# Performance work log

Measured on AMD Instinct MI355X. Metric: run time of the kernel, lower is better.

The kernel has to match this reference:

```python
import jax, jax.numpy as jnp
import numpy as np

N_SPOT, N_CITY, N_WORD = 20000, 2000, 20000
E_HAS, E_IN, E_DESC, E_RDESC = 100000, 100000, 400000, 400000
HID = 256


def setup_inputs() -> dict:
    key = jax.random.key(0)
    ks = jax.random.split(key, 48)

    def g(i, shape, s):
        return jax.random.normal(ks[i], shape, dtype=jnp.float32) * s

    inp = {}
    inp['x_spot'] = g(0, (N_SPOT, 2560), 0.5)
    inp['x_city'] = g(1, (N_CITY, 128), 0.5)
    inp['x_word'] = g(2, (N_WORD, 300), 0.5)
    inp['W_att'] = g(3, (4, 512, 128), 0.05)  # 4 heads, per_dim=128
    inp['q_att'] = g(4, (4, 128), 0.1)
    i = 5
    for n, d in [('w1_has_s', 128), ('w1_has_t', 512), ('w1_in_s', 512), ('w1_in_t', 128),
                 ('w1_desc_s', 300), ('w1_desc_t', 512), ('w1_rdesc_s', 512), ('w1_rdesc_t', 300)]:
        inp[n] = g(i, (d, HID), 0.05); i += 1
    for n in ['w2_has_s', 'w2_has_t', 'w2_in_s', 'w2_in_t', 'w2_desc_s', 'w2_desc_t', 'w2_rdesc_s', 'w2_rdesc_t']:
        inp[n] = g(i, (HID, HID), 0.05); i += 1
    for n in ['wl_spot', 'wl_city', 'wl_word']:
        inp[n] = g(i, (HID, 1), 0.05); i += 1
    for n in ['bl_spot', 'bl_city', 'bl_word']:
        inp[n] = jnp.zeros((1,), jnp.float32)
    for n, e, hi in [('e_has_src', E_HAS, N_CITY), ('e_has_tgt', E_HAS, N_SPOT),
                     ('e_in_src', E_IN, N_SPOT), ('e_in_tgt', E_IN, N_CITY),
                     ('e_desc_src', E_DESC, N_WORD), ('e_desc_tgt', E_DESC, N_SPOT),
                     ('e_rdesc_src', E_RDESC, N_SPOT), ('e_rdesc_tgt', E_RDESC, N_WORD)]:
        inp[n] = jax.random.randint(ks[i], (e,), 0, hi, dtype=jnp.int32); i += 1
    return inp


def _attention(x, W_att, q_att):
    # AttentionModule(input_dim=512, num_heads=4, split=5): (N, 2560) -> (N, 512)
    x = x.reshape(-1, 5, 512)
    xw = jnp.einsum('nsi,hio->hnso', x, W_att)                      # (4,N,5,128)
    a = jax.nn.leaky_relu(jnp.einsum('hnso,ho->hns', xw, q_att), 0.2)
    a = jax.nn.softmax(a, axis=2)                                   # softmax over split dim
    out = jnp.einsum('hnso,hns->hno', xw, a)                        # (4,N,128)
    return jnp.transpose(out, (1, 0, 2)).reshape(x.shape[0], 4 * 128)


def _scatter_mean(src, idx, n):
    s = jax.ops.segment_sum(src, idx, num_segments=n)
    c = jax.ops.segment_sum(jnp.ones((src.shape[0], 1), src.dtype), idx, num_segments=n)
    return s / jnp.maximum(c, 1.0)


def _edge(x_s, x_t, w_s, w_t, src, tgt):
    # per-edge-type linear, gather on source index, scatter-mean into targets
    msg = (x_s @ w_s)[src]
    return x_t @ w_t + _scatter_mean(msg, tgt, x_t.shape[0])


def _conv(xs, xc, xw, w, e):
    spot = _edge(xc, xs, w['has_s'], w['has_t'], e['has_src'], e['has_tgt']) \
         + _edge(xw, xs, w['desc_s'], w['desc_t'], e['desc_src'], e['desc_tgt'])
    city = _edge(xs, xc, w['in_s'], w['in_t'], e['in_src'], e['in_tgt'])
    word = _edge(xs, xw, w['rdesc_s'], w['rdesc_t'], e['rdesc_src'], e['rdesc_tgt'])
    # div[spot]=2, div[city]=div[word]=1; ReLU flag applies a second (idempotent) relu
    return jax.nn.relu(spot * 0.5), jax.nn.relu(city), jax.nn.relu(word)


def reference(x_spot, x_city, x_word, W_att, q_att,
              w1_has_s, w1_has_t, w1_in_s, w1_in_t, w1_desc_s, w1_desc_t, w1_rdesc_s, w1_rdesc_t,
              w2_has_s, w2_has_t, w2_in_s, w2_in_t, w2_desc_s, w2_desc_t, w2_rdesc_s, w2_rdesc_t,
              wl_spot, bl_spot, wl_city, bl_city, wl_word, bl_word,
              e_has_src, e_has_tgt, e_in_src, e_in_tgt, e_desc_src, e_desc_tgt, e_rdesc_src, e_rdesc_tgt):
    e = dict(has_src=e_has_src, has_tgt=e_has_tgt, in_src=e_in_src, in_tgt=e_in_tgt,
             desc_src=e_desc_src, desc_tgt=e_desc_tgt, rdesc_src=e_rdesc_src, rdesc_tgt=e_rdesc_tgt)
    w1 = dict(has_s=w1_has_s, has_t=w1_has_t, in_s=w1_in_s, in_t=w1_in_t,
              desc_s=w1_desc_s, desc_t=w1_desc_t, rdesc_s=w1_rdesc_s, rdesc_t=w1_rdesc_t)
    w2 = dict(has_s=w2_has_s, has_t=w2_has_t, in_s=w2_in_s, in_t=w2_in_t,
              desc_s=w2_desc_s, desc_t=w2_desc_t, rdesc_s=w2_rdesc_s, rdesc_t=w2_rdesc_t)
    xs = _attention(x_spot, W_att, q_att)  # multi=True path
    s1, c1, wd1 = _conv(xs, x_city, x_word, w1, e)
    s2, c2, wd2 = _conv(s1, c1, wd1, w2, e)
    out_spot = s2 @ wl_spot + bl_spot
    out_city = c2 @ wl_city + bl_city
    out_word = wd2 @ wl_word + bl_word
    # concat=True: mean over the two layer outputs per node type
    return ((s1 + s2) * 0.5, (c1 + c2) * 0.5, (wd1 + wd2) * 0.5, out_spot, out_city, out_word)
```

## Files before the change

kernel.cpp:

```cpp
#include <hip/hip_runtime.h>
#include <hip/hip_bf16.h>

#define HID 256
#define NSPOT 20000
#define NCITY 2000
#define NWORD 20000

typedef __attribute__((ext_vector_type(8))) short bhalf8;
typedef __attribute__((ext_vector_type(4))) float floatx4;
typedef __attribute__((ext_vector_type(8))) unsigned short ushortx8;

__device__ inline float bf2f(unsigned short u) {
    union { unsigned int i; float f; } v; v.i = (unsigned int)u << 16; return v.f;
}
__device__ inline unsigned short f2bf(float f) {
    __hip_bfloat16 b = __float2bfloat16(f);
    return *reinterpret_cast<unsigned short*>(&b);
}
__device__ inline float4 ld4(const float* p, size_t off) {
    return *reinterpret_cast<const float4*>(p + off);
}

__global__ void wq_kernel(const float* __restrict__ W, const float* __restrict__ q,
                          float* __restrict__ wq) {
    int idx = blockIdx.x * 256 + threadIdx.x;
    if (idx >= 2048) return;
    int h = idx >> 9, i = idx & 511;
    const float* Wr = W + ((size_t)h * 512 + i) * 128;
    const float* qr = q + h * 128;
    float s = 0.f;
    #pragma unroll 4
    for (int o = 0; o < 128; o++) s += Wr[o] * qr[o];
    wq[idx] = s;
}

__global__ __launch_bounds__(256) void attn_kernel(const float* __restrict__ x,
                                                   const float* __restrict__ wq,
                                                   __hip_bfloat16* __restrict__ xbar) {
    __shared__ float xl[2560];
    __shared__ float al[4][8];
    int n = blockIdx.x;
    int tid = threadIdx.x;
    int wave = tid >> 6, lane = tid & 63;
    const float4* xr4 = (const float4*)(x + (size_t)n * 2560);
    for (int i = tid; i < 640; i += 256) ((float4*)xl)[i] = xr4[i];
    __syncthreads();
    const float* wqh = wq + wave * 512;
    for (int s = 0; s < 5; s++) {
        float a = 0.f;
        #pragma unroll
        for (int j = 0; j < 8; j++)
            a += xl[s * 512 + lane + j * 64] * wqh[lane + j * 64];
        #pragma unroll
        for (int off = 32; off > 0; off >>= 1) a += __shfl_down(a, off, 64);
        if (lane == 0) al[wave][s] = a;
    }
    __syncthreads();
    if (tid < 4) {
        float z[5]; float m = -1e30f;
        #pragma unroll
        for (int s = 0; s < 5; s++) {
            float v = al[tid][s];
            v = (v >= 0.f) ? v : 0.2f * v;
            z[s] = v; m = fmaxf(m, v);
        }
        float e[5]; float sum = 0.f;
        #pragma unroll
        for (int s = 0; s < 5; s++) { e[s] = __expf(z[s] - m); sum += e[s]; }
        float r = 1.f / sum;
        #pragma unroll
        for (int s = 0; s < 5; s++) al[tid][s] = e[s] * r;
    }
    __syncthreads();
    float a0 = al[wave][0], a1 = al[wave][1], a2 = al[wave][2], a3 = al[wave][3], a4 = al[wave][4];
    __hip_bfloat16* xo = xbar + ((size_t)wave * NSPOT + n) * 512;
    #pragma unroll
    for (int j = 0; j < 8; j++) {
        int i = lane + j * 64;
        float v = a0 * xl[i] + a1 * xl[512 + i] + a2 * xl[1024 + i] + a3 * xl[1536 + i] + a4 * xl[2048 + i];
        xo[i] = __float2bfloat16(v);
    }
}

#define KP 40
struct GemmDesc {
    const __hip_bfloat16* A;
    const __hip_bfloat16* Bt;
    float* C;
    __hip_bfloat16* Cb;
    int lda, ldb, ldc, ldcb, M, K, N;
};
struct GemmDesc8 { GemmDesc d[8]; };

__global__ __launch_bounds__(256) void gemm_grouped(GemmDesc8 descs) {
    GemmDesc g = descs.d[blockIdx.z];
    int rowbase = blockIdx.x * 128;
    int colbase = blockIdx.y * 128;
    if (rowbase >= g.M || colbase >= g.N) return;
    __shared__ short As[128 * KP];
    __shared__ short Bs[128 * KP];
    int tid = threadIdx.x;
    int wave = tid >> 6, lane = tid & 63;
    int wr = wave & 1, wc = wave >> 1;
    int quad = lane >> 4, l16 = lane & 15;
    int srow = tid >> 2;
    int skoff = (tid & 3) * 8;
    const __hip_bfloat16* A = g.A;
    const __hip_bfloat16* Bt = g.Bt;
    int lda = g.lda, ldb = g.ldb, M = g.M, K = g.K;
    floatx4 acc[4][4];
    #pragma unroll
    for (int i = 0; i < 4; i++)
        #pragma unroll
        for (int j = 0; j < 4; j++)
            acc[i][j] = (floatx4){0.f, 0.f, 0.f, 0.f};

    for (int k0 = 0; k0 < K; k0 += 32) {
        #pragma unroll
        for (int i = 0; i < 2; i++) {
            int r = srow + i * 64;
            int gr = rowbase + r;
            int4 va = make_int4(0, 0, 0, 0);
            if (gr < M) va = *(const int4*)(A + (size_t)gr * lda + k0 + skoff);
            *(int4*)(As + r * KP + skoff) = va;
            int4 vb = *(const int4*)(Bt + (size_t)(colbase + r) * ldb + k0 + skoff);
            *(int4*)(Bs + r * KP + skoff) = vb;
        }
        __syncthreads();
        bhalf8 af[4], bfr[4];
        #pragma unroll
        for (int rt = 0; rt < 4; rt++)
            af[rt] = *(const bhalf8*)(As + (wr * 64 + rt * 16 + l16) * KP + quad * 8);
        #pragma unroll
        for (int ct = 0; ct < 4; ct++)
            bfr[ct] = *(const bhalf8*)(Bs + (wc * 64 + ct * 16 + l16) * KP + quad * 8);
        #pragma unroll
        for (int rt = 0; rt < 4; rt++)
            #pragma unroll
            for (int ct = 0; ct < 4; ct++)
                acc[rt][ct] = __builtin_amdgcn_mfma_f32_16x16x32_bf16(af[rt], bfr[ct], acc[rt][ct], 0, 0, 0);
        __syncthreads();
    }
    #pragma unroll
    for (int rt = 0; rt < 4; rt++) {
        #pragma unroll
        for (int r = 0; r < 4; r++) {
            int grow = rowbase + wr * 64 + rt * 16 + quad * 4 + r;
            if (grow < M) {
                #pragma unroll
                for (int ct = 0; ct < 4; ct++) {
                    int gcol = colbase + wc * 64 + ct * 16 + l16;
                    float v = acc[rt][ct][r];
                    if (g.C)  g.C[(size_t)grow * g.ldc + gcol] = v;
                    if (g.Cb) g.Cb[(size_t)grow * g.ldcb + gcol] = __float2bfloat16(v);
                }
            }
        }
    }
}

struct TDesc { const float* in; const float* in2; __hip_bfloat16* out; int K; int N; int Kp; };
struct TDesc8 { TDesc d[8]; };
__global__ void transpose_cast_kernel(TDesc8 descs) {
    TDesc dsc = descs.d[blockIdx.z];
    __shared__ float tile[32][33];
    int k0 = blockIdx.x * 32, n0 = blockIdx.y * 32;
    if (k0 >= dsc.Kp || n0 >= dsc.N) return;
    int tn = threadIdx.x & 31, t8 = threadIdx.x >> 5;
    #pragma unroll
    for (int i = 0; i < 4; i++) {
        int k = k0 + t8 * 4 + i;
        float v = 0.f;
        if (k < dsc.K && n0 + tn < dsc.N) {
            v = dsc.in[(size_t)k * dsc.N + n0 + tn];
            if (dsc.in2) v += dsc.in2[(size_t)k * dsc.N + n0 + tn];
        }
        tile[t8 * 4 + i][tn] = v;
    }
    __syncthreads();
    int kk = threadIdx.x & 31, n8 = threadIdx.x >> 5;
    #pragma unroll
    for (int i = 0; i < 4; i++) {
        int n = n0 + n8 * 4 + i;
        int k = k0 + kk;
        if (n < dsc.N && k < dsc.Kp)
            dsc.out[(size_t)n * dsc.Kp + k] = __float2bfloat16(tile[kk][n8 * 4 + i]);
    }
}

__global__ void cast_kernel(const float* __restrict__ in, __hip_bfloat16* __restrict__ out, int n) {
    int i = blockIdx.x * 256 + threadIdx.x;
    if (i < n) out[i] = __float2bfloat16(in[i]);
}

__global__ void cast_pad_kernel(const float* __restrict__ in, __hip_bfloat16* __restrict__ out,
                                int rows, int K, int Kp) {
    int idx = blockIdx.x * 256 + threadIdx.x;
    if (idx >= rows * Kp) return;
    int r = idx / Kp, k = idx - r * Kp;
    out[idx] = (k < K) ? __float2bfloat16(in[(size_t)r * K + k]) : __float2bfloat16(0.f);
}

struct EdgeDesc { const int* src; const int* tgt; int E; int n;
                  int* deg; int* rp; int* cur; int* cs; };
struct EdgeDesc4 { EdgeDesc d[4]; };

__global__ void hist4_kernel(EdgeDesc4 ds) {
    EdgeDesc d = ds.d[blockIdx.y];
    int e = blockIdx.x * 256 + threadIdx.x;
    if (e < d.E) atomicAdd(&d.deg[d.tgt[e]], 1);
}

__global__ void scan4_kernel(EdgeDesc4 ds) {
    EdgeDesc dd = ds.d[blockIdx.x];
    __shared__ int partx[257];
    __shared__ int part[256];
    int tid = threadIdx.x;
    int n = dd.n;
    int chunk = (n + 255) / 256;
    int lo = tid * chunk;
    int hi = lo + chunk; if (hi > n) hi = n;
    int s = 0;
    for (int i = lo; i < hi; i++) s += dd.deg[i];
    part[tid] = s;
    __syncthreads();
    if (tid == 0) {
        int acc = 0;
        for (int i = 0; i < 256; i++) { partx[i] = acc; acc += part[i]; }
        partx[256] = acc;
    }
    __syncthreads();
    int acc = partx[tid];
    for (int i = lo; i < hi; i++) { dd.rp[i] = acc; dd.cur[i] = acc; acc += dd.deg[i]; }
    if (tid == 0) dd.rp[n] = partx[256];
}

__global__ void fill4_kernel(EdgeDesc4 ds) {
    EdgeDesc d = ds.d[blockIdx.y];
    int e = blockIdx.x * 256 + threadIdx.x;
    if (e >= d.E) return;
    int t = d.tgt[e];
    int pos = atomicAdd(&d.cur[t], 1);
    d.cs[pos] = d.src[e];
}

__device__ inline void seg_mean8(const __hip_bfloat16* __restrict__ msg,
                                 const int* __restrict__ rp, const int* __restrict__ cs,
                                 int t, int half, int li, float a[8]) {
    int lo = rp[t], hi = rp[t + 1];
    #pragma unroll
    for (int j = 0; j < 8; j++) a[j] = 0.f;
    int col = li * 8;
    int i = lo + half;
    for (; i + 6 < hi; i += 8) {
        int s0 = cs[i], s1 = cs[i + 2], s2 = cs[i + 4], s3 = cs[i + 6];
        ushortx8 u0 = *(const ushortx8*)(msg + (size_t)s0 * HID + col);
        ushortx8 u1 = *(const ushortx8*)(msg + (size_t)s1 * HID + col);
        ushortx8 u2 = *(const ushortx8*)(msg + (size_t)s2 * HID + col);
        ushortx8 u3 = *(const ushortx8*)(msg + (size_t)s3 * HID + col);
        #pragma unroll
        for (int k = 0; k < 8; k++)
            a[k] += (bf2f(u0[k]) + bf2f(u1[k])) + (bf2f(u2[k]) + bf2f(u3[k]));
    }
    for (; i < hi; i += 2) {
        int s0 = cs[i];
        ushortx8 u = *(const ushortx8*)(msg + (size_t)s0 * HID + col);
        #pragma unroll
        for (int k = 0; k < 8; k++) a[k] += bf2f(u[k]);
    }
    #pragma unroll
    for (int j = 0; j < 8; j++) a[j] += __shfl_down(a[j], 32, 64);
    float inv = 1.f / fmaxf((float)(hi - lo), 1.f);
    #pragma unroll
    for (int j = 0; j < 8; j++) a[j] *= inv;
}

__global__ __launch_bounds__(256) void fused_ac1_kernel(
    const __hip_bfloat16* __restrict__ Phas,   const int* __restrict__ rp_has,   const int* __restrict__ cs_has,
    const __hip_bfloat16* __restrict__ Pdesc,  const int* __restrict__ rp_desc,  const int* __restrict__ cs_desc,
    const __hip_bfloat16* __restrict__ Pin,    const int* __restrict__ rp_in,    const int* __restrict__ cs_in,
    const __hip_bfloat16* __restrict__ Prdesc, const int* __restrict__ rp_rdesc, const int* __restrict__ cs_rdesc,
    const float* __restrict__ Ss, const float* __restrict__ Sc, const float* __restrict__ Sw,
    __hip_bfloat16* __restrict__ s1b, __hip_bfloat16* __restrict__ c1b,
    __hip_bfloat16* __restrict__ wd1b) {
    int row = blockIdx.x * 4 + (threadIdx.x >> 6);
    if (row >= NSPOT + NCITY + NWORD) return;
    int lane = threadIdx.x & 63;
    int half = lane >> 5, li = lane & 31;
    float v[8]; __hip_bfloat16* ob; size_t off;
    if (row < NSPOT) {
        float mh[8], md[8];
        seg_mean8(Phas, rp_has, cs_has, row, half, li, mh);
        seg_mean8(Pdesc, rp_desc, cs_desc, row, half, li, md);
        off = (size_t)row * HID + li * 8;
        float4 sa = ld4(Ss, off), sb = ld4(Ss, off + 4);
        v[0] = fmaxf((sa.x + mh[0] + md[0]) * 0.5f, 0.f);
        v[1] = fmaxf((sa.y + mh[1] + md[1]) * 0.5f, 0.f);
        v[2] = fmaxf((sa.z + mh[2] + md[2]) * 0.5f, 0.f);
        v[3] = fmaxf((sa.w + mh[3] + md[3]) * 0.5f, 0.f);
        v[4] = fmaxf((sb.x + mh[4] + md[4]) * 0.5f, 0.f);
        v[5] = fmaxf((sb.y + mh[5] + md[5]) * 0.5f, 0.f);
        v[6] = fmaxf((sb.z + mh[6] + md[6]) * 0.5f, 0.f);
        v[7] = fmaxf((sb.w + mh[7] + md[7]) * 0.5f, 0.f);
        ob = s1b;
    } else if (row < NSPOT + NCITY) {
        int r = row - NSPOT;
        float mi[8];
        seg_mean8(Pin, rp_in, cs_in, r, half, li, mi);
        off = (size_t)r * HID + li * 8;
        float4 sa = ld4(Sc, off), sb = ld4(Sc, off + 4);
        v[0] = fmaxf(sa.x + mi[0], 0.f); v[1] = fmaxf(sa.y + mi[1], 0.f);
        v[2] = fmaxf(sa.z + mi[2], 0.f); v[3] = fmaxf(sa.w + mi[3], 0.f);
        v[4] = fmaxf(sb.x + mi[4], 0.f); v[5] = fmaxf(sb.y + mi[5], 0.f);
        v[6] = fmaxf(sb.z + mi[6], 0.f); v[7] = fmaxf(sb.w + mi[7], 0.f);
        ob = c1b;
    } else {
        int r = row - NSPOT - NCITY;
        float mr[8];
        seg_mean8(Prdesc, rp_rdesc, cs_rdesc, r, half, li, mr);
        off = (size_t)r * HID + li * 8;
        float4 sa = ld4(Sw, off), sb = ld4(Sw, off + 4);
        v[0] = fmaxf(sa.x + mr[0], 0.f); v[1] = fmaxf(sa.y + mr[1], 0.f);
        v[2] = fmaxf(sa.z + mr[2], 0.f); v[3] = fmaxf(sa.w + mr[3], 0.f);
        v[4] = fmaxf(sb.x + mr[4], 0.f); v[5] = fmaxf(sb.y + mr[5], 0.f);
        v[6] = fmaxf(sb.z + mr[6], 0.f); v[7] = fmaxf(sb.w + mr[7], 0.f);
        ob = wd1b;
    }
    if (half == 0) {
        ushortx8 ub;
        #pragma unroll
        for (int j = 0; j < 8; j++) ub[j] = f2bf(v[j]);
        *reinterpret_cast<ushortx8*>((unsigned short*)ob + off) = ub;
    }
}

__global__ __launch_bounds__(256) void fused_finale_kernel(
    const __hip_bfloat16* __restrict__ Phas,   const int* __restrict__ rp_has,   const int* __restrict__ cs_has,
    const __hip_bfloat16* __restrict__ Pdesc,  const int* __restrict__ rp_desc,  const int* __restrict__ cs_desc,
    const __hip_bfloat16* __restrict__ Pin,    const int* __restrict__ rp_in,    const int* __restrict__ cs_in,
    const __hip_bfloat16* __restrict__ Prdesc, const int* __restrict__ rp_rdesc, const int* __restrict__ cs_rdesc,
    const float* __restrict__ Ss, const float* __restrict__ Sc, const float* __restrict__ Sw,
    const __hip_bfloat16* __restrict__ s1b, const __hip_bfloat16* __restrict__ c1b,
    const __hip_bfloat16* __restrict__ wd1b,
    float* __restrict__ out0, const float* __restrict__ wls, const float* __restrict__ bls, float* __restrict__ out3,
    float* __restrict__ out1, const float* __restrict__ wlc, const float* __restrict__ blc, float* __restrict__ out4,
    float* __restrict__ out2, const float* __restrict__ wlw, const float* __restrict__ blw, float* __restrict__ out5) {
    int row = blockIdx.x * 4 + (threadIdx.x >> 6);
    if (row >= NSPOT + NCITY + NWORD) return;
    int lane = threadIdx.x & 63;
    int half = lane >> 5, li = lane & 31;
    float v[8]; const __hip_bfloat16* pl; const float* wl; const float* bl;
    float* om; float* od;
    int r; size_t off;
    if (row < NSPOT) {
        r = row;
        float mh[8], md[8];
        seg_mean8(Phas, rp_has, cs_has, r, half, li, mh);
        seg_mean8(Pdesc, rp_desc, cs_desc, r, half, li, md);
        off = (size_t)r * HID + li * 8;
        float4 sa = ld4(Ss, off), sb = ld4(Ss, off + 4);
        v[0] = fmaxf((sa.x + mh[0] + md[0]) * 0.5f, 0.f);
        v[1] = fmaxf((sa.y + mh[1] + md[1]) * 0.5f, 0.f);
        v[2] = fmaxf((sa.z + mh[2] + md[2]) * 0.5f, 0.f);
        v[3] = fmaxf((sa.w + mh[3] + md[3]) * 0.5f, 0.f);
        v[4] = fmaxf((sb.x + mh[4] + md[4]) * 0.5f, 0.f);
        v[5] = fmaxf((sb.y + mh[5] + md[5]) * 0.5f, 0.f);
        v[6] = fmaxf((sb.z + mh[6] + md[6]) * 0.5f, 0.f);
        v[7] = fmaxf((sb.w + mh[7] + md[7]) * 0.5f, 0.f);
        pl = s1b; wl = wls; bl = bls; om = out0; od = out3;
    } else if (row < NSPOT + NCITY) {
        r = row - NSPOT;
        float mi[8];
        seg_mean8(Pin, rp_in, cs_in, r, half, li, mi);
        off = (size_t)r * HID + li * 8;
        float4 sa = ld4(Sc, off), sb = ld4(Sc, off + 4);
        v[0] = fmaxf(sa.x + mi[0], 0.f); v[1] = fmaxf(sa.y + mi[1], 0.f);
        v[2] = fmaxf(sa.z + mi[2], 0.f); v[3] = fmaxf(sa.w + mi[3], 0.f);
        v[4] = fmaxf(sb.x + mi[4], 0.f); v[5] = fmaxf(sb.y + mi[5], 0.f);
        v[6] = fmaxf(sb.z + mi[6], 0.f); v[7] = fmaxf(sb.w + mi[7], 0.f);
        pl = c1b; wl = wlc; bl = blc; om = out1; od = out4;
    } else {
        r = row - NSPOT - NCITY;
        float mr[8];
        seg_mean8(Prdesc, rp_rdesc, cs_rdesc, r, half, li, mr);
        off = (size_t)r * HID + li * 8;
        float4 sa = ld4(Sw, off), sb = ld4(Sw, off + 4);
        v[0] = fmaxf(sa.x + mr[0], 0.f); v[1] = fmaxf(sa.y + mr[1], 0.f);
        v[2] = fmaxf(sa.z + mr[2], 0.f); v[3] = fmaxf(sa.w + mr[3], 0.f);
        v[4] = fmaxf(sb.x + mr[4], 0.f); v[5] = fmaxf(sb.y + mr[5], 0.f);
        v[6] = fmaxf(sb.z + mr[6], 0.f); v[7] = fmaxf(sb.w + mr[7], 0.f);
        pl = wd1b; wl = wlw; bl = blw; om = out2; od = out5;
    }
    ushortx8 up = *(const ushortx8*)((const unsigned short*)pl + off);
    if (half == 0) {
        *reinterpret_cast<float4*>(om + off) =
            make_float4((bf2f(up[0]) + v[0]) * 0.5f, (bf2f(up[1]) + v[1]) * 0.5f,
                        (bf2f(up[2]) + v[2]) * 0.5f, (bf2f(up[3]) + v[3]) * 0.5f);
        *reinterpret_cast<float4*>(om + off + 4) =
            make_float4((bf2f(up[4]) + v[4]) * 0.5f, (bf2f(up[5]) + v[5]) * 0.5f,
                        (bf2f(up[6]) + v[6]) * 0.5f, (bf2f(up[7]) + v[7]) * 0.5f);
    }
    float4 wa = *reinterpret_cast<const float4*>(wl + li * 8);
    float4 wb = *reinterpret_cast<const float4*>(wl + li * 8 + 4);
    float s = v[0] * wa.x + v[1] * wa.y + v[2] * wa.z + v[3] * wa.w
            + v[4] * wb.x + v[5] * wb.y + v[6] * wb.z + v[7] * wb.w;
    s += __shfl_down(s, 16, 64);
    s += __shfl_down(s, 8, 64);
    s += __shfl_down(s, 4, 64);
    s += __shfl_down(s, 2, 64);
    s += __shfl_down(s, 1, 64);
    if (lane == 0) od[r] = s + bl[0];
}

extern "C" void kernel_launch(void* const* d_in, const int* in_sizes, int n_in,
                              void* d_out, int out_size, void* d_ws, size_t ws_size,
                              hipStream_t stream) {
    const float* x_spot   = (const float*)d_in[0];
    const float* x_city   = (const float*)d_in[1];
    const float* x_word   = (const float*)d_in[2];
    const float* W_att    = (const float*)d_in[3];
    const float* q_att    = (const float*)d_in[4];
    const float* w1[8] = { (const float*)d_in[5], (const float*)d_in[6], (const float*)d_in[7],
                           (const float*)d_in[8], (const float*)d_in[9], (const float*)d_in[10],
                           (const float*)d_in[11], (const float*)d_in[12] };
    const float* w2[8] = { (const float*)d_in[13], (const float*)d_in[14], (const float*)d_in[15],
                           (const float*)d_in[16], (const float*)d_in[17], (const float*)d_in[18],
                           (const float*)d_in[19], (const float*)d_in[20] };
    const float* wl_spot = (const float*)d_in[21];
    const float* wl_city = (const float*)d_in[22];
    const float* wl_word = (const float*)d_in[23];
    const float* bl_spot = (const float*)d_in[24];
    const float* bl_city = (const float*)d_in[25];
    const float* bl_word = (const float*)d_in[26];
    const int* e_has_src   = (const int*)d_in[27];
    const int* e_has_tgt   = (const int*)d_in[28];
    const int* e_in_src    = (const int*)d_in[29];
    const int* e_in_tgt    = (const int*)d_in[30];
    const int* e_desc_src  = (const int*)d_in[31];
    const int* e_desc_tgt  = (const int*)d_in[32];
    const int* e_rdesc_src = (const int*)d_in[33];
    const int* e_rdesc_tgt = (const int*)d_in[34];
    const int E_has   = in_sizes[27];
    const int E_in    = in_sizes[29];
    const int E_desc  = in_sizes[31];
    const int E_rdesc = in_sizes[33];

    float* out = (float*)d_out;
    float* wsf = (float*)d_ws;
    typedef __hip_bfloat16 bf;

    size_t o = 0;
    auto alloc = [&](size_t nfloats) { float* p = wsf + o; o += (nfloats + 15) & ~(size_t)15; return p; };
    float* wqb       = alloc(2048);
    bf* xs_bf        = (bf*)alloc((size_t)NSPOT * 512 / 2);
    bf* x_city_bf    = (bf*)alloc((size_t)NCITY * 128 / 2);
    bf* x_word_bf    = (bf*)alloc((size_t)NWORD * 320 / 2);
    bf* Wt_att       = (bf*)alloc((size_t)4 * 128 * 512 / 2);
    int Kp1[7] = {128, 512, 512, 128, 320, 512, 320};
    bf* Wt1[7];
    for (int i = 0; i < 7; i++) Wt1[i] = (bf*)alloc((size_t)256 * Kp1[i] / 2);
    bf* Wt2[7];
    for (int i = 0; i < 7; i++) Wt2[i] = (bf*)alloc((size_t)256 * 256 / 2);
    float* Ss = alloc((size_t)NSPOT * HID);
    float* Sc = alloc((size_t)NCITY * HID);
    float* Sw = alloc((size_t)NWORD * HID);
    size_t regX = o;
    bf* xbar_bf = (bf*)(wsf + regX);
    size_t ox = regX;
    auto allocX = [&](size_t nfloats) { float* p = wsf + ox; ox += (nfloats + 15) & ~(size_t)15; return p; };
    bf* P_has_bf   = (bf*)allocX((size_t)NCITY * HID / 2);
    bf* P_in_bf    = (bf*)allocX((size_t)NSPOT * HID / 2);
    bf* P_desc_bf  = (bf*)allocX((size_t)NWORD * HID / 2);
    bf* P_rdesc_bf = (bf*)allocX((size_t)NSPOT * HID / 2);
    bf* s1b = (bf*)allocX((size_t)NSPOT * HID / 2);
    bf* c1b = (bf*)allocX((size_t)NCITY * HID / 2);
    bf* wd1b = (bf*)allocX((size_t)NWORD * HID / 2);
    o = regX + (size_t)4 * NSPOT * 512 / 2;
    int* wsi = (int*)(wsf + o);
    size_t io = 0;
    int* deg_has    = wsi + io; io += NSPOT;
    int* deg_desc   = wsi + io; io += NSPOT;
    int* deg_in     = wsi + io; io += NCITY;
    int* deg_rdesc  = wsi + io; io += NWORD;
    size_t deg_bytes = io * sizeof(int);
    int* rp_has     = wsi + io; io += NSPOT + 1;
    int* rp_desc    = wsi + io; io += NSPOT + 1;
    int* rp_in      = wsi + io; io += NCITY + 1;
    int* rp_rdesc   = wsi + io; io += NWORD + 1;
    int* cur_has    = wsi + io; io += NSPOT + 1;
    int* cur_desc   = wsi + io; io += NSPOT + 1;
    int* cur_in     = wsi + io; io += NCITY + 1;
    int* cur_rdesc  = wsi + io; io += NWORD + 1;
    int* cs_has     = wsi + io; io += E_has;
    int* cs_desc    = wsi + io; io += E_desc;
    int* cs_in      = wsi + io; io += E_in;
    int* cs_rdesc   = wsi + io; io += E_rdesc;
    (void)ws_size; (void)n_in; (void)out_size;

    {
        TDesc8 t{};
        for (int i = 0; i < 4; i++)
            t.d[i] = TDesc{ W_att + (size_t)i * 512 * 128, nullptr,
                            Wt_att + (size_t)i * 128 * 512, 512, 128, 512 };
        hipLaunchKernelGGL(transpose_cast_kernel, dim3(16, 4, 4), dim3(256), 0, stream, t);
    }
    {
        TDesc8 t{};
        t.d[0] = TDesc{ w1[0], nullptr, Wt1[0], 128, 256, 128 };
        t.d[1] = TDesc{ w1[1], w1[5],   Wt1[1], 512, 256, 512 };
        t.d[2] = TDesc{ w1[2], nullptr, Wt1[2], 512, 256, 512 };
        t.d[3] = TDesc{ w1[3], nullptr, Wt1[3], 128, 256, 128 };
        t.d[4] = TDesc{ w1[4], nullptr, Wt1[4], 300, 256, 320 };
        t.d[5] = TDesc{ w1[6], nullptr, Wt1[5], 512, 256, 512 };
        t.d[6] = TDesc{ w1[7], nullptr, Wt1[6], 300, 256, 320 };
        hipLaunchKernelGGL(transpose_cast_kernel, dim3(16, 8, 8), dim3(256), 0, stream, t);
    }
    {
        TDesc8 t{};
        t.d[0] = TDesc{ w2[0], nullptr, Wt2[0], 256, 256, 256 };
        t.d[1] = TDesc{ w2[1], w2[5],   Wt2[1], 256, 256, 256 };
        t.d[2] = TDesc{ w2[2], nullptr, Wt2[2], 256, 256, 256 };
        t.d[3] = TDesc{ w2[3], nullptr, Wt2[3], 256, 256, 256 };
        t.d[4] = TDesc{ w2[4], nullptr, Wt2[4], 256, 256, 256 };
        t.d[5] = TDesc{ w2[6], nullptr, Wt2[5], 256, 256, 256 };
        t.d[6] = TDesc{ w2[7], nullptr, Wt2[6], 256, 256, 256 };
        hipLaunchKernelGGL(transpose_cast_kernel, dim3(8, 8, 8), dim3(256), 0, stream, t);
    }
    hipLaunchKernelGGL(cast_kernel, dim3((NCITY * 128 + 255) / 256), dim3(256), 0, stream,
                       x_city, x_city_bf, NCITY * 128);
    hipLaunchKernelGGL(cast_pad_kernel, dim3((NWORD * 320 + 255) / 256), dim3(256), 0, stream,
                       x_word, x_word_bf, NWORD, 300, 320);

    EdgeDesc4 ed;
    ed.d[0] = EdgeDesc{ e_has_src,   e_has_tgt,   E_has,   NSPOT, deg_has,   rp_has,   cur_has,   cs_has };
    ed.d[1] = EdgeDesc{ e_desc_src,  e_desc_tgt,  E_desc,  NSPOT, deg_desc,  rp_desc,  cur_desc,  cs_desc };
    ed.d[2] = EdgeDesc{ e_in_src,    e_in_tgt,    E_in,    NCITY, deg_in,    rp_in,    cur_in,    cs_in };
    ed.d[3] = EdgeDesc{ e_rdesc_src, e_rdesc_tgt, E_rdesc, NWORD, deg_rdesc, rp_rdesc, cur_rdesc, cs_rdesc };
    int Emax = E_has;
    if (E_desc > Emax) Emax = E_desc;
    if (E_in > Emax) Emax = E_in;
    if (E_rdesc > Emax) Emax = E_rdesc;
    hipMemsetAsync((void*)deg_has, 0, deg_bytes, stream);
    hipLaunchKernelGGL(hist4_kernel, dim3((Emax + 255) / 256, 4), dim3(256), 0, stream, ed);
    hipLaunchKernelGGL(scan4_kernel, dim3(4), dim3(256), 0, stream, ed);
    hipLaunchKernelGGL(fill4_kernel, dim3((Emax + 255) / 256, 4), dim3(256), 0, stream, ed);

    hipLaunchKernelGGL(wq_kernel, dim3(8), dim3(256), 0, stream, W_att, q_att, wqb);
    hipLaunchKernelGGL(attn_kernel, dim3(NSPOT), dim3(256), 0, stream, x_spot, wqb, xbar_bf);

    int gx = (NSPOT + 127) / 128;

    {
        GemmDesc8 gd{};
        for (int h = 0; h < 4; h++)
            gd.d[h] = GemmDesc{ xbar_bf + (size_t)h * NSPOT * 512, Wt_att + (size_t)h * 128 * 512,
                                nullptr, xs_bf + h * 128, 512, 512, 0, 512, NSPOT, 512, 128 };
        hipLaunchKernelGGL(gemm_grouped, dim3(gx, 1, 4), dim3(256), 0, stream, gd);
    }

    {
        GemmDesc8 gd{};
        gd.d[0] = GemmDesc{ x_city_bf, Wt1[0], nullptr, P_has_bf,   128, 128, 0, HID, NCITY, 128, HID };
        gd.d[1] = GemmDesc{ xs_bf,     Wt1[1], Ss,      nullptr,    512, 512, HID, 0, NSPOT, 512, HID };
        gd.d[2] = GemmDesc{ xs_bf,     Wt1[2], nullptr, P_in_bf,    512, 512, 0, HID, NSPOT, 512, HID };
        gd.d[3] = GemmDesc{ x_city_bf, Wt1[3], Sc,      nullptr,    128, 128, HID, 0, NCITY, 128, HID };
        gd.d[4] = GemmDesc{ x_word_bf, Wt1[4], nullptr, P_desc_bf,  320, 320, 0, HID, NWORD, 320, HID };
        gd.d[5] = GemmDesc{ xs_bf,     Wt1[5], nullptr, P_rdesc_bf, 512, 512, 0, HID, NSPOT, 512, HID };
        gd.d[6] = GemmDesc{ x_word_bf, Wt1[6], Sw,      nullptr,    320, 320, HID, 0, NWORD, 320, HID };
        gd.d[7].M = 0; gd.d[7].N = 0;
        hipLaunchKernelGGL(gemm_grouped, dim3(gx, 2, 8), dim3(256), 0, stream, gd);
    }

    int rows3 = NSPOT + NCITY + NWORD;
    hipLaunchKernelGGL(fused_ac1_kernel, dim3((rows3 + 3) / 4), dim3(256), 0, stream,
                       P_has_bf, rp_has, cs_has, P_desc_bf, rp_desc, cs_desc,
                       P_in_bf, rp_in, cs_in, P_rdesc_bf, rp_rdesc, cs_rdesc,
                       Ss, Sc, Sw, s1b, c1b, wd1b);

    {
        GemmDesc8 gd{};
        gd.d[0] = GemmDesc{ c1b,  Wt2[0], nullptr, P_has_bf,   HID, HID, 0, HID, NCITY, HID, HID };
        gd.d[1] = GemmDesc{ s1b,  Wt2[1], Ss,      nullptr,    HID, HID, HID, 0, NSPOT, HID, HID };
        gd.d[2] = GemmDesc{ s1b,  Wt2[2], nullptr, P_in_bf,    HID, HID, 0, HID, NSPOT, HID, HID };
        gd.d[3] = GemmDesc{ c1b,  Wt2[3], Sc,      nullptr,    HID, HID, HID, 0, NCITY, HID, HID };
        gd.d[4] = GemmDesc{ wd1b, Wt2[4], nullptr, P_desc_bf,  HID, HID, 0, HID, NWORD, HID, HID };
        gd.d[5] = GemmDesc{ s1b,  Wt2[5], nullptr, P_rdesc_bf, HID, HID, 0, HID, NSPOT, HID, HID };
        gd.d[6] = GemmDesc{ wd1b, Wt2[6], Sw,      nullptr,    HID, HID, HID, 0, NWORD, HID, HID };
        gd.d[7].M = 0; gd.d[7].N = 0;
        hipLaunchKernelGGL(gemm_grouped, dim3(gx, 2, 8), dim3(256), 0, stream, gd);
    }

    float* out0 = out;
    float* out1 = out + (size_t)NSPOT * HID;
    float* out2 = out1 + (size_t)NCITY * HID;
    float* out3 = out2 + (size_t)NWORD * HID;
    float* out4 = out3 + NSPOT;
    float* out5 = out4 + NCITY;
    hipLaunchKernelGGL(fused_finale_kernel, dim3((rows3 + 3) / 4), dim3(256), 0, stream,
                       P_has_bf, rp_has, cs_has, P_desc_bf, rp_desc, cs_desc,
                       P_in_bf, rp_in, cs_in, P_rdesc_bf, rp_rdesc, cs_rdesc,
                       Ss, Sc, Sw, s1b, c1b, wd1b,
                       out0, wl_spot, bl_spot, out3,
                       out1, wl_city, bl_city, out4,
                       out2, wl_word, bl_word, out5);
}
```

Baseline: 835.1 us.

## Merge weight transposes into one launch and rebalance grouped GEMM launches

The three weight transpose-cast launches are merged into a single launch with 18 descriptors. The city and word layer-1 GEMMs move into the attention-projection grouped GEMM, which does not depend on xs, so that launch is better filled and the following launch holds only the three spot GEMMs. P_has and P_desc move out of the aliased xbar region so they are not overwritten while xbar is still live. The GEMM tile loader now precomputes row pointers and clamps out-of-range A rows to M-1 instead of zero-filling them, which removes per-iteration branches and index math; the extra rows are never stored.

```diff
diff --git a/kernel.cpp b/kernel.cpp
--- a/kernel.cpp
+++ b/kernel.cpp
@@ -108,6 +108,19 @@
     const __hip_bfloat16* A = g.A;
     const __hip_bfloat16* Bt = g.Bt;
     int lda = g.lda, ldb = g.ldb, M = g.M, K = g.K;
+
+    int r0 = srow, r1 = srow + 64;
+    int gra0 = rowbase + r0; gra0 = gra0 < M ? gra0 : M - 1;
+    int gra1 = rowbase + r1; gra1 = gra1 < M ? gra1 : M - 1;
+    const __hip_bfloat16* Arow0 = A + (size_t)gra0 * lda + skoff;
+    const __hip_bfloat16* Arow1 = A + (size_t)gra1 * lda + skoff;
+    const __hip_bfloat16* Brow0 = Bt + (size_t)(colbase + r0) * ldb + skoff;
+    const __hip_bfloat16* Brow1 = Bt + (size_t)(colbase + r1) * ldb + skoff;
+    short* sA0 = As + r0 * KP + skoff;
+    short* sA1 = As + r1 * KP + skoff;
+    short* sB0 = Bs + r0 * KP + skoff;
+    short* sB1 = Bs + r1 * KP + skoff;
+
     floatx4 acc[4][4];
     #pragma unroll
     for (int i = 0; i < 4; i++)
@@ -116,16 +129,10 @@
             acc[i][j] = (floatx4){0.f, 0.f, 0.f, 0.f};
 
     for (int k0 = 0; k0 < K; k0 += 32) {
-        #pragma unroll
-        for (int i = 0; i < 2; i++) {
-            int r = srow + i * 64;
-            int gr = rowbase + r;
-            int4 va = make_int4(0, 0, 0, 0);
-            if (gr < M) va = *(const int4*)(A + (size_t)gr * lda + k0 + skoff);
-            *(int4*)(As + r * KP + skoff) = va;
-            int4 vb = *(const int4*)(Bt + (size_t)(colbase + r) * ldb + k0 + skoff);
-            *(int4*)(Bs + r * KP + skoff) = vb;
-        }
+        *(int4*)sA0 = *(const int4*)(Arow0 + k0);
+        *(int4*)sA1 = *(const int4*)(Arow1 + k0);
+        *(int4*)sB0 = *(const int4*)(Brow0 + k0);
+        *(int4*)sB1 = *(const int4*)(Brow1 + k0);
         __syncthreads();
         bhalf8 af[4], bfr[4];
         #pragma unroll
@@ -160,8 +167,8 @@
 }
 
 struct TDesc { const float* in; const float* in2; __hip_bfloat16* out; int K; int N; int Kp; };
-struct TDesc8 { TDesc d[8]; };
-__global__ void transpose_cast_kernel(TDesc8 descs) {
+struct TDesc18 { TDesc d[18]; };
+__global__ void transpose_cast_kernel(TDesc18 descs) {
     TDesc dsc = descs.d[blockIdx.z];
     __shared__ float tile[32][33];
     int k0 = blockIdx.x * 32, n0 = blockIdx.y * 32;
@@ -464,13 +471,13 @@
     float* Ss = alloc((size_t)NSPOT * HID);
     float* Sc = alloc((size_t)NCITY * HID);
     float* Sw = alloc((size_t)NWORD * HID);
+    bf* P_has_bf  = (bf*)alloc((size_t)NCITY * HID / 2);
+    bf* P_desc_bf = (bf*)alloc((size_t)NWORD * HID / 2);
     size_t regX = o;
     bf* xbar_bf = (bf*)(wsf + regX);
     size_t ox = regX;
     auto allocX = [&](size_t nfloats) { float* p = wsf + ox; ox += (nfloats + 15) & ~(size_t)15; return p; };
-    bf* P_has_bf   = (bf*)allocX((size_t)NCITY * HID / 2);
     bf* P_in_bf    = (bf*)allocX((size_t)NSPOT * HID / 2);
-    bf* P_desc_bf  = (bf*)allocX((size_t)NWORD * HID / 2);
     bf* P_rdesc_bf = (bf*)allocX((size_t)NSPOT * HID / 2);
     bf* s1b = (bf*)allocX((size_t)NSPOT * HID / 2);
     bf* c1b = (bf*)allocX((size_t)NCITY * HID / 2);
@@ -498,33 +505,25 @@
     (void)ws_size; (void)n_in; (void)out_size;
 
     {
-        TDesc8 t{};
+        TDesc18 t{};
         for (int i = 0; i < 4; i++)
             t.d[i] = TDesc{ W_att + (size_t)i * 512 * 128, nullptr,
                             Wt_att + (size_t)i * 128 * 512, 512, 128, 512 };
-        hipLaunchKernelGGL(transpose_cast_kernel, dim3(16, 4, 4), dim3(256), 0, stream, t);
-    }
-    {
-        TDesc8 t{};
-        t.d[0] = TDesc{ w1[0], nullptr, Wt1[0], 128, 256, 128 };
-        t.d[1] = TDesc{ w1[1], w1[5],   Wt1[1], 512, 256, 512 };
-        t.d[2] = TDesc{ w1[2], nullptr, Wt1[2], 512, 256, 512 };
-        t.d[3] = TDesc{ w1[3], nullptr, Wt1[3], 128, 256, 128 };
-        t.d[4] = TDesc{ w1[4], nullptr, Wt1[4], 300, 256, 320 };
-        t.d[5] = TDesc{ w1[6], nullptr, Wt1[5], 512, 256, 512 };
-        t.d[6] = TDesc{ w1[7], nullptr, Wt1[6], 300, 256, 320 };
-        hipLaunchKernelGGL(transpose_cast_kernel, dim3(16, 8, 8), dim3(256), 0, stream, t);
-    }
-    {
-        TDesc8 t{};
-        t.d[0] = TDesc{ w2[0], nullptr, Wt2[0], 256, 256, 256 };
-        t.d[1] = TDesc{ w2[1], w2[5],   Wt2[1], 256, 256, 256 };
-        t.d[2] = TDesc{ w2[2], nullptr, Wt2[2], 256, 256, 256 };
-        t.d[3] = TDesc{ w2[3], nullptr, Wt2[3], 256, 256, 256 };
-        t.d[4] = TDesc{ w2[4], nullptr, Wt2[4], 256, 256, 256 };
-        t.d[5] = TDesc{ w2[6], nullptr, Wt2[5], 256, 256, 256 };
-        t.d[6] = TDesc{ w2[7], nullptr, Wt2[6], 256, 256, 256 };
-        hipLaunchKernelGGL(transpose_cast_kernel, dim3(8, 8, 8), dim3(256), 0, stream, t);
+        t.d[4]  = TDesc{ w1[0], nullptr, Wt1[0], 128, 256, 128 };
+        t.d[5]  = TDesc{ w1[1], w1[5],   Wt1[1], 512, 256, 512 };
+        t.d[6]  = TDesc{ w1[2], nullptr, Wt1[2], 512, 256, 512 };
+        t.d[7]  = TDesc{ w1[3], nullptr, Wt1[3], 128, 256, 128 };
+        t.d[8]  = TDesc{ w1[4], nullptr, Wt1[4], 300, 256, 320 };
+        t.d[9]  = TDesc{ w1[6], nullptr, Wt1[5], 512, 256, 512 };
+        t.d[10] = TDesc{ w1[7], nullptr, Wt1[6], 300, 256, 320 };
+        t.d[11] = TDesc{ w2[0], nullptr, Wt2[0], 256, 256, 256 };
+        t.d[12] = TDesc{ w2[1], w2[5],   Wt2[1], 256, 256, 256 };
+        t.d[13] = TDesc{ w2[2], nullptr, Wt2[2], 256, 256, 256 };
+        t.d[14] = TDesc{ w2[3], nullptr, Wt2[3], 256, 256, 256 };
+        t.d[15] = TDesc{ w2[4], nullptr, Wt2[4], 256, 256, 256 };
+        t.d[16] = TDesc{ w2[6], nullptr, Wt2[5], 256, 256, 256 };
+        t.d[17] = TDesc{ w2[7], nullptr, Wt2[6], 256, 256, 256 };
+        hipLaunchKernelGGL(transpose_cast_kernel, dim3(16, 8, 18), dim3(256), 0, stream, t);
     }
     hipLaunchKernelGGL(cast_kernel, dim3((NCITY * 128 + 255) / 256), dim3(256), 0, stream,
                        x_city, x_city_bf, NCITY * 128);
@@ -555,20 +554,20 @@
         for (int h = 0; h < 4; h++)
             gd.d[h] = GemmDesc{ xbar_bf + (size_t)h * NSPOT * 512, Wt_att + (size_t)h * 128 * 512,
                                 nullptr, xs_bf + h * 128, 512, 512, 0, 512, NSPOT, 512, 128 };
-        hipLaunchKernelGGL(gemm_grouped, dim3(gx, 1, 4), dim3(256), 0, stream, gd);
+        gd.d[4] = GemmDesc{ x_city_bf, Wt1[0], nullptr, P_has_bf,  128, 128, 0, HID, NCITY, 128, HID };
+        gd.d[5] = GemmDesc{ x_city_bf, Wt1[3], Sc,      nullptr,   128, 128, HID, 0, NCITY, 128, HID };
+        gd.d[6] = GemmDesc{ x_word_bf, Wt1[4], nullptr, P_desc_bf, 320, 320, 0, HID, NWORD, 320, HID };
+        gd.d[7] = GemmDesc{ x_word_bf, Wt1[6], Sw,      nullptr,   320, 320, HID, 0, NWORD, 320, HID };
+        hipLaunchKernelGGL(gemm_grouped, dim3(gx, 2, 8), dim3(256), 0, stream, gd);
     }
 
     {
         GemmDesc8 gd{};
-        gd.d[0] = GemmDesc{ x_city_bf, Wt1[0], nullptr, P_has_bf,   128, 128, 0, HID, NCITY, 128, HID };
-        gd.d[1] = GemmDesc{ xs_bf,     Wt1[1], Ss,      nullptr,    512, 512, HID, 0, NSPOT, 512, HID };
-        gd.d[2] = GemmDesc{ xs_bf,     Wt1[2], nullptr, P_in_bf,    512, 512, 0, HID, NSPOT, 512, HID };
-        gd.d[3] = GemmDesc{ x_city_bf, Wt1[3], Sc,      nullptr,    128, 128, HID, 0, NCITY, 128, HID };
-        gd.d[4] = GemmDesc{ x_word_bf, Wt1[4], nullptr, P_desc_bf,  320, 320, 0, HID, NWORD, 320, HID };
-        gd.d[5] = GemmDesc{ xs_bf,     Wt1[5], nullptr, P_rdesc_bf, 512, 512, 0, HID, NSPOT, 512, HID };
-        gd.d[6] = GemmDesc{ x_word_bf, Wt1[6], Sw,      nullptr,    320, 320, HID, 0, NWORD, 320, HID };
-        gd.d[7].M = 0; gd.d[7].N = 0;
-        hipLaunchKernelGGL(gemm_grouped, dim3(gx, 2, 8), dim3(256), 0, stream, gd);
+        gd.d[0] = GemmDesc{ xs_bf, Wt1[1], Ss,      nullptr,    512, 512, HID, 0, NSPOT, 512, HID };
+        gd.d[1] = GemmDesc{ xs_bf, Wt1[2], nullptr, P_in_bf,    512, 512, 0, HID, NSPOT, 512, HID };
+        gd.d[2] = GemmDesc{ xs_bf, Wt1[5], nullptr, P_rdesc_bf, 512, 512, 0, HID, NSPOT, 512, HID };
+        for (int i = 3; i < 8; i++) { gd.d[i].M = 0; gd.d[i].N = 0; }
+        hipLaunchKernelGGL(gemm_grouped, dim3(gx, 2, 3), dim3(256), 0, stream, gd);
     }
 
     int rows3 = NSPOT + NCITY + NWORD;
```

Measured after the change: 819.4 us. No clear change (-1.9%).
